# Kernel optimization log

Hardware: AMD Instinct MI355X
Metric: run time of the kernel (lower is better)

The kernel has to match this reference:

```python
import jax, jax.numpy as jnp
import numpy as np

R, S, C, HID = 8192, 128, 32, 64   # rays, samples/ray, grid_chn, mlp_hidden_chn
G = 128                            # voxel grid resolution
COLOR_CHN = 3
NUM_HARM = 3
OPACITY_INIT_BIAS = -5.0
GAIN = 1.0
HE_DIM = 3 * 2 * NUM_HARM + 3      # harmonic embedding dim = 21

def _relu(x):
    return jnp.maximum(x, 0.0)

def _trilinear(grid, p):
    # grid: [G, G, G, Cg] indexed [z, y, x]; p: [N, 3] xyz coords in [-1, 1]
    g = grid.shape[0]
    c = (p + 1.0) * 0.5 * (g - 1)  # align_corners=True convention
    c0f = jnp.floor(c)
    fr = c - c0f
    c0 = jnp.clip(c0f.astype(jnp.int32), 0, g - 1)
    c1 = jnp.clip(c0 + 1, 0, g - 1)
    x0, y0, z0 = c0[:, 0], c0[:, 1], c0[:, 2]
    x1, y1, z1 = c1[:, 0], c1[:, 1], c1[:, 2]
    fx, fy, fz = fr[:, 0:1], fr[:, 1:2], fr[:, 2:3]
    out = jnp.zeros((p.shape[0], grid.shape[-1]), grid.dtype)
    for xi, wx in ((x0, 1.0 - fx), (x1, fx)):
        for yi, wy in ((y0, 1.0 - fy), (y1, fy)):
            for zi, wz in ((z0, 1.0 - fz), (z1, fz)):
                out = out + (wx * wy * wz) * grid[zi, yi, xi]
    return out

def _harmonic(d):
    # [sin(2^i d), cos(2^i d)] for i<NUM_HARM, with raw direction appended
    freqs = 2.0 ** jnp.arange(NUM_HARM, dtype=jnp.float32)
    ang = d[:, None, :] * freqs[None, :, None]  # [R, NH, 3]
    n = d.shape[0]
    return jnp.concatenate([jnp.sin(ang).reshape(n, -1), jnp.cos(ang).reshape(n, -1), d], axis=-1)

def _forward(origins, directions, near, far, feature_grid, Wr, br, Wt1, bt1, Wt2, bt2, Wo1, bo1, Wo2, bo2, Wc1, bc1, Wc2, bc2):
    n_rays = origins.shape[0]
    # stratified midpoints between near and far
    t = near[:, None] + (far - near)[:, None] * (jnp.arange(S, dtype=jnp.float32) + 0.5) / S
    pts = origins[:, None, :] + t[..., None] * directions[:, None, :]  # [R, S, 3]
    feats = _trilinear(feature_grid, pts.reshape(-1, 3)).reshape(n_rays, S, -1)
    # trunk MLP
    e = _relu(feats @ Wt1 + bt1)
    e = _relu(e @ Wt2 + bt2)
    # opacity MLP (last-layer bias carries opacity_init_bias)
    raw = _relu(e @ Wo1 + bo1) @ Wo2 + bo2  # [R, S, 1]
    density = jax.nn.softplus(GAIN * raw[..., 0])
    delta = ((far - near) / S)[:, None]
    alpha = 1.0 - jnp.exp(-delta * density)  # [R, S]
    trans = jnp.cumprod(1.0 - alpha, axis=1)
    T = jnp.concatenate([jnp.ones((n_rays, 1), alpha.dtype), trans[:, :-1]], axis=1)
    w = T * alpha  # compositing weights
    # color branch: harmonic ray-direction encoding added to color-MLP input
    ray_enc = _harmonic(directions) @ Wr + br  # [R, HID]
    cin = e + ray_enc[:, None, :]
    col = jax.nn.sigmoid(_relu(cin @ Wc1 + bc1) @ Wc2 + bc2)  # [R, S, COLOR_CHN]
    color = jnp.einsum('rs,rsc->rc', w, col)
    mask = 1.0 - trans[:, -1]
    color = color + (1.0 - mask)[:, None] * 0.0  # bg_color = 0.0
    return color, mask

def setup_inputs():
    key = jax.random.key(0)
    ks = jax.random.split(key, 16)
    directions = jax.random.normal(ks[0], (R, 3), jnp.float32)
    directions = directions / jnp.linalg.norm(directions, axis=-1, keepdims=True)
    origins = jnp.zeros((R, 3), jnp.float32)
    near = jnp.full((R,), 0.1, jnp.float32)
    far = jnp.full((R,), 1.0, jnp.float32)
    feature_grid = jax.random.normal(ks[1], (G, G, G, C), jnp.float32) * 0.1
    def lin(k, i, o):
        s = (2.0 / (i + o)) ** 0.5
        return jax.random.normal(k, (i, o), jnp.float32) * s
    return {
        'origins': origins, 'directions': directions, 'near': near, 'far': far,
        'feature_grid': feature_grid,
        'Wr': lin(ks[2], HE_DIM, HID), 'br': jnp.zeros((HID,), jnp.float32),
        'Wt1': lin(ks[3], C, HID), 'bt1': jnp.zeros((HID,), jnp.float32),
        'Wt2': lin(ks[4], HID, HID), 'bt2': jnp.zeros((HID,), jnp.float32),
        'Wo1': lin(ks[5], HID, HID), 'bo1': jnp.zeros((HID,), jnp.float32),
        'Wo2': lin(ks[6], HID, 1), 'bo2': jnp.full((1,), OPACITY_INIT_BIAS, jnp.float32),
        'Wc1': lin(ks[7], HID, HID), 'bc1': jnp.zeros((HID,), jnp.float32),
        'Wc2': lin(ks[8], HID, COLOR_CHN), 'bc2': jnp.zeros((COLOR_CHN,), jnp.float32),
    }

def reference(origins, directions, near, far, feature_grid, Wr, br, Wt1, bt1, Wt2, bt2, Wo1, bo1, Wo2, bo2, Wc1, bc1, Wc2, bc2):
    return _forward(origins, directions, near, far, feature_grid, Wr, br, Wt1, bt1, Wt2, bt2, Wo1, bo1, Wo2, bo2, Wc1, bc1, Wc2, bc2)
```

## Files before the change

### kernel.cpp

```cpp
#include <hip/hip_runtime.h>
#include <math.h>

#define NRAYS 8192
#define XPAD 72

typedef short s16x8 __attribute__((ext_vector_type(8)));
typedef float f32x4 __attribute__((ext_vector_type(4)));

__device__ __forceinline__ unsigned short f2bf(float x){
  unsigned u = __float_as_uint(x);
  u += 0x7FFF + ((u >> 16) & 1);
  return (unsigned short)(u >> 16);
}
__device__ __forceinline__ float bf2f(unsigned short s){ return __uint_as_float(((unsigned)s) << 16); }
__device__ __forceinline__ float softplusf_(float x){ return (x > 20.f) ? x : log1pf(expf(x)); }
__device__ __forceinline__ float sigmoidf_(float x){ return 1.f / (1.f + expf(-x)); }

__global__ void prep_weights(const float* __restrict__ Wt1, const float* __restrict__ Wt2,
                             const float* __restrict__ Wo1, const float* __restrict__ Wc1,
                             unsigned short* __restrict__ ws)
{
  const int i0 = blockIdx.x * blockDim.x + threadIdx.x;
  const int st = gridDim.x * blockDim.x;
  for (int i = i0; i < 2048; i += st){ int n = i >> 5, k = i & 31; ws[i]         = f2bf(Wt1[k * 64 + n]); }
  for (int i = i0; i < 4096; i += st){ int n = i >> 6, k = i & 63; ws[2048 + i]  = f2bf(Wt2[k * 64 + n]); }
  for (int i = i0; i < 4096; i += st){ int n = i >> 6, k = i & 63; ws[6144 + i]  = f2bf(Wo1[k * 64 + n]); }
  for (int i = i0; i < 4096; i += st){ int n = i >> 6, k = i & 63; ws[10240 + i] = f2bf(Wc1[k * 64 + n]); }
}

__device__ __forceinline__ void layer64(const s16x8 a[4][2], const unsigned short* __restrict__ wt,
                                        const float* __restrict__ bias, int ln15, int quad,
                                        f32x4 acc[4][4])
{
  float bv[4];
#pragma unroll
  for (int nt = 0; nt < 4; ++nt) bv[nt] = bias[nt * 16 + ln15];
#pragma unroll
  for (int mt = 0; mt < 4; ++mt)
#pragma unroll
    for (int nt = 0; nt < 4; ++nt){ f32x4 c; c[0] = bv[nt]; c[1] = bv[nt]; c[2] = bv[nt]; c[3] = bv[nt]; acc[mt][nt] = c; }
#pragma unroll
  for (int ks = 0; ks < 2; ++ks){
    s16x8 b[4];
#pragma unroll
    for (int nt = 0; nt < 4; ++nt)
      b[nt] = *(const s16x8*)(wt + (nt * 16 + ln15) * 64 + ks * 32 + quad * 8);
#pragma unroll
    for (int mt = 0; mt < 4; ++mt)
#pragma unroll
      for (int nt = 0; nt < 4; ++nt)
        acc[mt][nt] = __builtin_amdgcn_mfma_f32_16x16x32_bf16(a[mt][ks], b[nt], acc[mt][nt], 0, 0, 0);
  }
}

__device__ __forceinline__ void store_relu(unsigned short* __restrict__ sX, int wrow, int ln15, int quad,
                                           const f32x4 acc[4][4])
{
#pragma unroll
  for (int mt = 0; mt < 4; ++mt){
    const int rowb = wrow + mt * 16 + quad * 4;
#pragma unroll
    for (int nt = 0; nt < 4; ++nt){
      const int col = nt * 16 + ln15;
#pragma unroll
      for (int r = 0; r < 4; ++r)
        sX[(rowb + r) * XPAD + col] = f2bf(fmaxf(acc[mt][nt][r], 0.f));
    }
  }
}

extern "C" __global__ __launch_bounds__(256, 2)
void lightplane_fwd(const float* __restrict__ origins, const float* __restrict__ dirs,
                    const float* __restrict__ nearv,   const float* __restrict__ farv,
                    const float* __restrict__ grid,
                    const float* __restrict__ Wr,  const float* __restrict__ br,
                    const float* __restrict__ bt1, const float* __restrict__ bt2,
                    const float* __restrict__ bo1,
                    const float* __restrict__ Wo2, const float* __restrict__ bo2,
                    const float* __restrict__ bc1,
                    const float* __restrict__ Wc2, const float* __restrict__ bc2,
                    const unsigned short* __restrict__ ws,
                    float* __restrict__ out)
{
  __shared__ unsigned short s_X[256 * XPAD];
  __shared__ float s_scan[2][128];
  __shared__ float s_enc[2][64];
  __shared__ float s_part[2][2][4];

  const int tid   = threadIdx.x;
  const int lane  = tid & 63;
  const int wv    = tid >> 6;
  const int ln15  = lane & 15, quad = lane >> 4;
  const int wrow  = wv * 64;
  const int r_loc = tid >> 7;
  const int s_idx = tid & 127;
  const int ray   = blockIdx.x * 2 + r_loc;

  if (tid < 128) {
    const int rr = tid >> 6, j = tid & 63;
    const int rg = blockIdx.x * 2 + rr;
    const float ddx = dirs[rg * 3 + 0], ddy = dirs[rg * 3 + 1], ddz = dirs[rg * 3 + 2];
    float h[21]; float f = 1.f;
#pragma unroll
    for (int q = 0; q < 3; ++q) {
      h[q * 3 + 0] = sinf(ddx * f); h[q * 3 + 1] = sinf(ddy * f); h[q * 3 + 2] = sinf(ddz * f);
      h[9 + q * 3 + 0] = cosf(ddx * f); h[9 + q * 3 + 1] = cosf(ddy * f); h[9 + q * 3 + 2] = cosf(ddz * f);
      f *= 2.f;
    }
    h[18] = ddx; h[19] = ddy; h[20] = ddz;
    float a = br[j];
#pragma unroll
    for (int i = 0; i < 21; ++i) a = fmaf(h[i], Wr[i * 64 + j], a);
    s_enc[rr][j] = a;
  }

  const float dx = dirs[ray * 3 + 0], dy = dirs[ray * 3 + 1], dz = dirs[ray * 3 + 2];
  const float ox = origins[ray * 3 + 0], oy = origins[ray * 3 + 1], oz = origins[ray * 3 + 2];
  const float nr = nearv[ray], fa = farv[ray];
  const float t  = nr + (fa - nr) * ((s_idx + 0.5f) * (1.0f / 128.0f));
  const float px = fmaf(t, dx, ox), py = fmaf(t, dy, oy), pz = fmaf(t, dz, oz);

  const float cx = (px + 1.f) * 63.5f, cy = (py + 1.f) * 63.5f, cz = (pz + 1.f) * 63.5f;
  const float fx0 = floorf(cx), fy0 = floorf(cy), fz0 = floorf(cz);
  const float frx = cx - fx0, fry = cy - fy0, frz = cz - fz0;
  int ix0 = min(max((int)fx0, 0), 127), iy0 = min(max((int)fy0, 0), 127), iz0 = min(max((int)fz0, 0), 127);
  int ix1 = min(ix0 + 1, 127), iy1 = min(iy0 + 1, 127), iz1 = min(iz0 + 1, 127);
  const float wxs[2] = {1.f - frx, frx}, wys[2] = {1.f - fry, fry}, wzs[2] = {1.f - frz, frz};
  const int xi[2] = {ix0, ix1}, yi[2] = {iy0, iy1}, zi[2] = {iz0, iz1};

  float fe[32];
#pragma unroll
  for (int k = 0; k < 32; ++k) fe[k] = 0.f;
#pragma unroll
  for (int a = 0; a < 2; ++a)
#pragma unroll
    for (int b2 = 0; b2 < 2; ++b2)
#pragma unroll
      for (int c2 = 0; c2 < 2; ++c2) {
        const float wgt = wzs[a] * wys[b2] * wxs[c2];
        const float4* g4 = (const float4*)(grid + ((size_t)((zi[a] * 128 + yi[b2]) * 128 + xi[c2])) * 32);
#pragma unroll
        for (int k = 0; k < 8; ++k) {
          float4 g = g4[k];
          fe[4 * k + 0] = fmaf(wgt, g.x, fe[4 * k + 0]);
          fe[4 * k + 1] = fmaf(wgt, g.y, fe[4 * k + 1]);
          fe[4 * k + 2] = fmaf(wgt, g.z, fe[4 * k + 2]);
          fe[4 * k + 3] = fmaf(wgt, g.w, fe[4 * k + 3]);
        }
      }

#pragma unroll
  for (int q = 0; q < 4; ++q) {
    s16x8 v;
#pragma unroll
    for (int j = 0; j < 8; ++j) v[j] = (short)f2bf(fe[q * 8 + j]);
    *(s16x8*)&s_X[tid * XPAD + q * 8] = v;
  }

  f32x4 acc[4][4];

  {
    s16x8 a1[4];
#pragma unroll
    for (int mt = 0; mt < 4; ++mt)
      a1[mt] = *(const s16x8*)&s_X[(wrow + mt * 16 + ln15) * XPAD + quad * 8];
    float bv[4];
#pragma unroll
    for (int nt = 0; nt < 4; ++nt) bv[nt] = bt1[nt * 16 + ln15];
#pragma unroll
    for (int mt = 0; mt < 4; ++mt)
#pragma unroll
      for (int nt = 0; nt < 4; ++nt){ f32x4 c; c[0]=bv[nt];c[1]=bv[nt];c[2]=bv[nt];c[3]=bv[nt]; acc[mt][nt]=c; }
    s16x8 b[4];
#pragma unroll
    for (int nt = 0; nt < 4; ++nt)
      b[nt] = *(const s16x8*)(ws + (nt * 16 + ln15) * 32 + quad * 8);
#pragma unroll
    for (int mt = 0; mt < 4; ++mt)
#pragma unroll
      for (int nt = 0; nt < 4; ++nt)
        acc[mt][nt] = __builtin_amdgcn_mfma_f32_16x16x32_bf16(a1[mt], b[nt], acc[mt][nt], 0, 0, 0);
    store_relu(s_X, wrow, ln15, quad, acc);
  }

  {
    s16x8 a[4][2];
#pragma unroll
    for (int ks = 0; ks < 2; ++ks)
#pragma unroll
      for (int mt = 0; mt < 4; ++mt)
        a[mt][ks] = *(const s16x8*)&s_X[(wrow + mt * 16 + ln15) * XPAD + ks * 32 + quad * 8];
    layer64(a, ws + 2048, bt2, ln15, quad, acc);
    store_relu(s_X, wrow, ln15, quad, acc);
  }

  s16x8 ea[4][2];
#pragma unroll
  for (int ks = 0; ks < 2; ++ks)
#pragma unroll
    for (int mt = 0; mt < 4; ++mt)
      ea[mt][ks] = *(const s16x8*)&s_X[(wrow + mt * 16 + ln15) * XPAD + ks * 32 + quad * 8];

  layer64(ea, ws + 6144, bo1, ln15, quad, acc);
  store_relu(s_X, wrow, ln15, quad, acc);
  float raw = bo2[0];
#pragma unroll
  for (int q = 0; q < 8; ++q) {
    s16x8 v = *(const s16x8*)&s_X[tid * XPAD + q * 8];
#pragma unroll
    for (int j = 0; j < 8; ++j)
      raw = fmaf(bf2f((unsigned short)v[j]), Wo2[q * 8 + j], raw);
  }
  const float density = softplusf_(raw);
  const float delta   = (fa - nr) * (1.0f / 128.0f);
  const float alpha   = 1.f - expf(-delta * density);

  __syncthreads();

  {
    s16x8 a[4][2];
#pragma unroll
    for (int ks = 0; ks < 2; ++ks) {
      const float* ep = &s_enc[r_loc][ks * 32 + quad * 8];
      float4 e0 = *(const float4*)ep;
      float4 e1 = *(const float4*)(ep + 4);
      float encv[8] = {e0.x, e0.y, e0.z, e0.w, e1.x, e1.y, e1.z, e1.w};
#pragma unroll
      for (int mt = 0; mt < 4; ++mt) {
        s16x8 v;
#pragma unroll
        for (int j = 0; j < 8; ++j)
          v[j] = (short)f2bf(bf2f((unsigned short)ea[mt][ks][j]) + encv[j]);
        a[mt][ks] = v;
      }
    }
    layer64(a, ws + 10240, bc1, ln15, quad, acc);
    store_relu(s_X, wrow, ln15, quad, acc);
  }
  float c0 = bc2[0], c1 = bc2[1], c2 = bc2[2];
#pragma unroll
  for (int q = 0; q < 8; ++q) {
    s16x8 v = *(const s16x8*)&s_X[tid * XPAD + q * 8];
#pragma unroll
    for (int j = 0; j < 8; ++j) {
      const float h = bf2f((unsigned short)v[j]);
      c0 = fmaf(h, Wc2[(q * 8 + j) * 3 + 0], c0);
      c1 = fmaf(h, Wc2[(q * 8 + j) * 3 + 1], c1);
      c2 = fmaf(h, Wc2[(q * 8 + j) * 3 + 2], c2);
    }
  }
  c0 = sigmoidf_(c0); c1 = sigmoidf_(c1); c2 = sigmoidf_(c2);

  float vv = 1.f - alpha;
  s_scan[r_loc][s_idx] = vv;
  __syncthreads();
#pragma unroll
  for (int off = 1; off < 128; off <<= 1) {
    const float u = (s_idx >= off) ? s_scan[r_loc][s_idx - off] : 1.f;
    __syncthreads();
    vv *= u;
    s_scan[r_loc][s_idx] = vv;
    __syncthreads();
  }
  const float Texcl = (s_idx == 0) ? 1.f : s_scan[r_loc][s_idx - 1];
  const float wgt = Texcl * alpha;

  float p0 = wgt * c0, p1 = wgt * c1, p2 = wgt * c2;
#pragma unroll
  for (int off = 32; off > 0; off >>= 1) {
    p0 += __shfl_down(p0, off, 64);
    p1 += __shfl_down(p1, off, 64);
    p2 += __shfl_down(p2, off, 64);
  }
  if ((tid & 63) == 0) {
    const int wvi = s_idx >> 6;
    s_part[r_loc][wvi][0] = p0; s_part[r_loc][wvi][1] = p1; s_part[r_loc][wvi][2] = p2;
  }
  __syncthreads();
  if (s_idx == 0) {
    out[ray * 3 + 0] = s_part[r_loc][0][0] + s_part[r_loc][1][0];
    out[ray * 3 + 1] = s_part[r_loc][0][1] + s_part[r_loc][1][1];
    out[ray * 3 + 2] = s_part[r_loc][0][2] + s_part[r_loc][1][2];
    out[NRAYS * 3 + ray] = 1.f - s_scan[r_loc][127];
  }
}

extern "C" void kernel_launch(void* const* d_in, const int* in_sizes, int n_in,
                              void* d_out, int out_size, void* d_ws, size_t ws_size,
                              hipStream_t stream)
{
  (void)in_sizes; (void)n_in; (void)out_size; (void)ws_size;
  const float* origins = (const float*)d_in[0];
  const float* dirs    = (const float*)d_in[1];
  const float* nearv   = (const float*)d_in[2];
  const float* farv    = (const float*)d_in[3];
  const float* grid    = (const float*)d_in[4];
  const float* Wr  = (const float*)d_in[5];
  const float* br  = (const float*)d_in[6];
  const float* Wt1 = (const float*)d_in[7];
  const float* bt1 = (const float*)d_in[8];
  const float* Wt2 = (const float*)d_in[9];
  const float* bt2 = (const float*)d_in[10];
  const float* Wo1 = (const float*)d_in[11];
  const float* bo1 = (const float*)d_in[12];
  const float* Wo2 = (const float*)d_in[13];
  const float* bo2 = (const float*)d_in[14];
  const float* Wc1 = (const float*)d_in[15];
  const float* bc1 = (const float*)d_in[16];
  const float* Wc2 = (const float*)d_in[17];
  const float* bc2 = (const float*)d_in[18];
  unsigned short* ws = (unsigned short*)d_ws;
  float* out = (float*)d_out;

  prep_weights<<<16, 256, 0, stream>>>(Wt1, Wt2, Wo1, Wc1, ws);
  lightplane_fwd<<<NRAYS / 2, 256, 0, stream>>>(origins, dirs, nearv, farv, grid,
                                                Wr, br, bt1, bt2, bo1, Wo2, bo2,
                                                bc1, Wc2, bc2, ws, out);
}
```

Measured before the change: 509.4 us.

## Sort rays by direction bucket, swizzle blocks, and use wave-shuffle transmittance scan

```diff
diff --git a/kernel.cpp b/kernel.cpp
--- a/kernel.cpp
+++ b/kernel.cpp
@@ -3,6 +3,8 @@
 
 #define NRAYS 8192
 #define XPAD 72
+
+#define WS_PERM_BYTE 28672
 
 typedef short s16x8 __attribute__((ext_vector_type(8)));
 typedef float f32x4 __attribute__((ext_vector_type(4)));
@@ -28,6 +30,32 @@
   for (int i = i0; i < 4096; i += st){ int n = i >> 6, k = i & 63; ws[10240 + i] = f2bf(Wc1[k * 64 + n]); }
 }
 
+__global__ __launch_bounds__(1024) void sort_rays(const float* __restrict__ dirs,
+                                                  int* __restrict__ perm)
+{
+  __shared__ int h[64];
+  __shared__ unsigned char keys[NRAYS];
+  const int tid = threadIdx.x;
+  if (tid < 64) h[tid] = 0;
+  __syncthreads();
+  for (int r = tid; r < NRAYS; r += 1024){
+    const float dx = dirs[3*r], dy = dirs[3*r+1], dz = dirs[3*r+2];
+    const int qx = min(3, max(0, (int)((dx + 1.f) * 2.f)));
+    const int qy = min(3, max(0, (int)((dy + 1.f) * 2.f)));
+    const int qz = min(3, max(0, (int)((dz + 1.f) * 2.f)));
+    const int k = (qx << 4) | (qy << 2) | qz;
+    keys[r] = (unsigned char)k;
+    atomicAdd(&h[k], 1);
+  }
+  __syncthreads();
+  if (tid == 0){ int s = 0; for (int i = 0; i < 64; ++i){ int c = h[i]; h[i] = s; s += c; } }
+  __syncthreads();
+  for (int r = tid; r < NRAYS; r += 1024){
+    const int pos = atomicAdd(&h[keys[r]], 1);
+    perm[pos] = r;
+  }
+}
+
 __device__ __forceinline__ void layer64(const s16x8 a[4][2], const unsigned short* __restrict__ wt,
                                         const float* __restrict__ bias, int ln15, int quad,
                                         f32x4 acc[4][4])
@@ -69,7 +97,7 @@
   }
 }
 
-extern "C" __global__ __launch_bounds__(256, 2)
+extern "C" __global__ __launch_bounds__(256, 4)
 void lightplane_fwd(const float* __restrict__ origins, const float* __restrict__ dirs,
                     const float* __restrict__ nearv,   const float* __restrict__ farv,
                     const float* __restrict__ grid,
@@ -80,12 +108,13 @@
                     const float* __restrict__ bc1,
                     const float* __restrict__ Wc2, const float* __restrict__ bc2,
                     const unsigned short* __restrict__ ws,
+                    const int* __restrict__ perm,
                     float* __restrict__ out)
 {
   __shared__ unsigned short s_X[256 * XPAD];
-  __shared__ float s_scan[2][128];
   __shared__ float s_enc[2][64];
   __shared__ float s_part[2][2][4];
+  __shared__ float s_wtot[4];
 
   const int tid   = threadIdx.x;
   const int lane  = tid & 63;
@@ -94,25 +123,10 @@
   const int wrow  = wv * 64;
   const int r_loc = tid >> 7;
   const int s_idx = tid & 127;
-  const int ray   = blockIdx.x * 2 + r_loc;
-
-  if (tid < 128) {
-    const int rr = tid >> 6, j = tid & 63;
-    const int rg = blockIdx.x * 2 + rr;
-    const float ddx = dirs[rg * 3 + 0], ddy = dirs[rg * 3 + 1], ddz = dirs[rg * 3 + 2];
-    float h[21]; float f = 1.f;
-#pragma unroll
-    for (int q = 0; q < 3; ++q) {
-      h[q * 3 + 0] = sinf(ddx * f); h[q * 3 + 1] = sinf(ddy * f); h[q * 3 + 2] = sinf(ddz * f);
-      h[9 + q * 3 + 0] = cosf(ddx * f); h[9 + q * 3 + 1] = cosf(ddy * f); h[9 + q * 3 + 2] = cosf(ddz * f);
-      f *= 2.f;
-    }
-    h[18] = ddx; h[19] = ddy; h[20] = ddz;
-    float a = br[j];
-#pragma unroll
-    for (int i = 0; i < 21; ++i) a = fmaf(h[i], Wr[i * 64 + j], a);
-    s_enc[rr][j] = a;
-  }
+
+  const int bid = (int)blockIdx.x;
+  const int wg  = (bid & 7) * ((int)gridDim.x >> 3) + (bid >> 3);
+  const int ray = perm[wg * 2 + r_loc];
 
   const float dx = dirs[ray * 3 + 0], dy = dirs[ray * 3 + 1], dz = dirs[ray * 3 + 2];
   const float ox = origins[ray * 3 + 0], oy = origins[ray * 3 + 1], oz = origins[ray * 3 + 2];
@@ -131,23 +145,28 @@
   float fe[32];
 #pragma unroll
   for (int k = 0; k < 32; ++k) fe[k] = 0.f;
-#pragma unroll
-  for (int a = 0; a < 2; ++a)
-#pragma unroll
-    for (int b2 = 0; b2 < 2; ++b2)
-#pragma unroll
-      for (int c2 = 0; c2 < 2; ++c2) {
-        const float wgt = wzs[a] * wys[b2] * wxs[c2];
-        const float4* g4 = (const float4*)(grid + ((size_t)((zi[a] * 128 + yi[b2]) * 128 + xi[c2])) * 32);
-#pragma unroll
-        for (int k = 0; k < 8; ++k) {
-          float4 g = g4[k];
-          fe[4 * k + 0] = fmaf(wgt, g.x, fe[4 * k + 0]);
-          fe[4 * k + 1] = fmaf(wgt, g.y, fe[4 * k + 1]);
-          fe[4 * k + 2] = fmaf(wgt, g.z, fe[4 * k + 2]);
-          fe[4 * k + 3] = fmaf(wgt, g.w, fe[4 * k + 3]);
-        }
+
+  const float4* __restrict__ gb = (const float4*)grid;
+#pragma unroll
+  for (int zz = 0; zz < 2; ++zz)
+#pragma unroll
+    for (int yy = 0; yy < 2; ++yy) {
+      const size_t rowb = (size_t)((zi[zz] * 128 + yi[yy]) * 128) * 8;
+      const float4* p0 = gb + rowb + (size_t)xi[0] * 8;
+      const float4* p1 = gb + rowb + (size_t)xi[1] * 8;
+      float4 v0[8], v1[8];
+#pragma unroll
+      for (int q = 0; q < 8; ++q) { v0[q] = p0[q]; v1[q] = p1[q]; }
+      const float wzy = wzs[zz] * wys[yy];
+      const float wA = wzy * wxs[0], wB = wzy * wxs[1];
+#pragma unroll
+      for (int q = 0; q < 8; ++q) {
+        fe[q * 4 + 0] = fmaf(wA, v0[q].x, fmaf(wB, v1[q].x, fe[q * 4 + 0]));
+        fe[q * 4 + 1] = fmaf(wA, v0[q].y, fmaf(wB, v1[q].y, fe[q * 4 + 1]));
+        fe[q * 4 + 2] = fmaf(wA, v0[q].z, fmaf(wB, v1[q].z, fe[q * 4 + 2]));
+        fe[q * 4 + 3] = fmaf(wA, v0[q].w, fmaf(wB, v1[q].w, fe[q * 4 + 3]));
       }
+    }
 
 #pragma unroll
   for (int q = 0; q < 4; ++q) {
@@ -155,6 +174,24 @@
 #pragma unroll
     for (int j = 0; j < 8; ++j) v[j] = (short)f2bf(fe[q * 8 + j]);
     *(s16x8*)&s_X[tid * XPAD + q * 8] = v;
+  }
+
+  if (tid < 128) {
+    const int rr = tid >> 6, j = tid & 63;
+    const int rg = perm[wg * 2 + rr];
+    const float ddx = dirs[rg * 3 + 0], ddy = dirs[rg * 3 + 1], ddz = dirs[rg * 3 + 2];
+    float h[21]; float f = 1.f;
+#pragma unroll
+    for (int q = 0; q < 3; ++q) {
+      h[q * 3 + 0] = sinf(ddx * f); h[q * 3 + 1] = sinf(ddy * f); h[q * 3 + 2] = sinf(ddz * f);
+      h[9 + q * 3 + 0] = cosf(ddx * f); h[9 + q * 3 + 1] = cosf(ddy * f); h[9 + q * 3 + 2] = cosf(ddz * f);
+      f *= 2.f;
+    }
+    h[18] = ddx; h[19] = ddy; h[20] = ddz;
+    float a = br[j];
+#pragma unroll
+    for (int i = 0; i < 21; ++i) a = fmaf(h[i], Wr[i * 64 + j], a);
+    s_enc[rr][j] = a;
   }
 
   f32x4 acc[4][4];
@@ -251,19 +288,19 @@
   }
   c0 = sigmoidf_(c0); c1 = sigmoidf_(c1); c2 = sigmoidf_(c2);
 
-  float vv = 1.f - alpha;
-  s_scan[r_loc][s_idx] = vv;
-  __syncthreads();
-#pragma unroll
-  for (int off = 1; off < 128; off <<= 1) {
-    const float u = (s_idx >= off) ? s_scan[r_loc][s_idx - off] : 1.f;
-    __syncthreads();
-    vv *= u;
-    s_scan[r_loc][s_idx] = vv;
-    __syncthreads();
-  }
-  const float Texcl = (s_idx == 0) ? 1.f : s_scan[r_loc][s_idx - 1];
-  const float wgt = Texcl * alpha;
+  float sc = 1.f - alpha;
+#pragma unroll
+  for (int off = 1; off < 64; off <<= 1) {
+    const float u = __shfl_up(sc, off, 64);
+    if (lane >= off) sc *= u;
+  }
+  float excl = __shfl_up(sc, 1, 64);
+  if (lane == 0) excl = 1.f;
+  if (lane == 63) s_wtot[wv] = sc;
+  __syncthreads();
+  const int w_in_ray = s_idx >> 6;
+  const float prefix = w_in_ray ? s_wtot[r_loc * 2] : 1.f;
+  const float wgt = prefix * excl * alpha;
 
   float p0 = wgt * c0, p1 = wgt * c1, p2 = wgt * c2;
 #pragma unroll
@@ -272,16 +309,15 @@
     p1 += __shfl_down(p1, off, 64);
     p2 += __shfl_down(p2, off, 64);
   }
-  if ((tid & 63) == 0) {
-    const int wvi = s_idx >> 6;
-    s_part[r_loc][wvi][0] = p0; s_part[r_loc][wvi][1] = p1; s_part[r_loc][wvi][2] = p2;
+  if (lane == 0) {
+    s_part[r_loc][w_in_ray][0] = p0; s_part[r_loc][w_in_ray][1] = p1; s_part[r_loc][w_in_ray][2] = p2;
   }
   __syncthreads();
   if (s_idx == 0) {
     out[ray * 3 + 0] = s_part[r_loc][0][0] + s_part[r_loc][1][0];
     out[ray * 3 + 1] = s_part[r_loc][0][1] + s_part[r_loc][1][1];
     out[ray * 3 + 2] = s_part[r_loc][0][2] + s_part[r_loc][1][2];
-    out[NRAYS * 3 + ray] = 1.f - s_scan[r_loc][127];
+    out[NRAYS * 3 + ray] = 1.f - s_wtot[r_loc * 2] * s_wtot[r_loc * 2 + 1];
   }
 }
 
@@ -310,10 +346,12 @@
   const float* Wc2 = (const float*)d_in[17];
   const float* bc2 = (const float*)d_in[18];
   unsigned short* ws = (unsigned short*)d_ws;
+  int* perm = (int*)((char*)d_ws + WS_PERM_BYTE);
   float* out = (float*)d_out;
 
   prep_weights<<<16, 256, 0, stream>>>(Wt1, Wt2, Wo1, Wc1, ws);
+  sort_rays<<<1, 1024, 0, stream>>>(dirs, perm);
   lightplane_fwd<<<NRAYS / 2, 256, 0, stream>>>(origins, dirs, nearv, farv, grid,
                                                 Wr, br, bt1, bt2, bo1, Wo2, bo2,
-                                                bc1, Wc2, bc2, ws, out);
-}
+                                                bc1, Wc2, bc2, ws, perm, out);
+}
```

New measurement: 553.2 us. 1.09x slower.
